# Optimization experiments

Hardware: AMD Instinct MI355X
Metric: run time of the kernel (lower is better)

Reference implementation:

```python
import jax, jax.numpy as jnp
import numpy as np

# Static module config (must match init_kwargs / input_specs)
C, HEADS, POINTS, LEVELS = 256, 8, 8, 2
H, W = 128, 128           # BEV grid per agent/level
NQ = H * W                # num_query = H*W
DH = C // HEADS           # per-head dim


def setup_inputs() -> dict:
    key = jax.random.key(0)
    ks = jax.random.split(key, 12)
    s = 0.02
    return {
        "query": jax.random.normal(ks[0], (1, NQ, C), jnp.float32),
        "query_pos": jax.random.normal(ks[1], (1, NQ, C), jnp.float32),
        "value": jax.random.normal(ks[2], (LEVELS, NQ, C), jnp.float32),
        "reference_points": jax.random.uniform(ks[3], (1, NQ, LEVELS, 2), jnp.float32),
        "spatial_shapes": jnp.full((LEVELS, 2), H, dtype=jnp.int32),
        "W_off": jax.random.normal(ks[4], (C, LEVELS * HEADS * POINTS * 2), jnp.float32) * s,
        "b_off": jax.random.normal(ks[5], (LEVELS * HEADS * POINTS * 2,), jnp.float32) * s,
        "W_attn": jax.random.normal(ks[6], (C, LEVELS * HEADS * POINTS), jnp.float32) * s,
        "b_attn": jax.random.normal(ks[7], (LEVELS * HEADS * POINTS,), jnp.float32) * s,
        "W_val": jax.random.normal(ks[8], (C, C), jnp.float32) * s,
        "b_val": jax.random.normal(ks[9], (C,), jnp.float32) * s,
        "W_out": jax.random.normal(ks[10], (C, C), jnp.float32) * s,
        "b_out": jax.random.normal(ks[11], (C,), jnp.float32) * s,
    }


def _bilinear(img, x, y):
    """grid_sample-style bilinear, align_corners=False, zero padding.
    img: (H, W, D); x, y: (...) pixel-space coords. Returns (..., D)."""
    Hh, Ww = img.shape[0], img.shape[1]
    x0f, y0f = jnp.floor(x), jnp.floor(y)
    x0, y0 = x0f.astype(jnp.int32), y0f.astype(jnp.int32)
    x1, y1 = x0 + 1, y0 + 1
    wx1, wy1 = x - x0f, y - y0f
    wx0, wy0 = 1.0 - wx1, 1.0 - wy1

    def gather(yy, xx):
        valid = (yy >= 0) & (yy < Hh) & (xx >= 0) & (xx < Ww)
        g = img[jnp.clip(yy, 0, Hh - 1), jnp.clip(xx, 0, Ww - 1)]
        return jnp.where(valid[..., None], g, 0.0)

    return (gather(y0, x0) * (wy0 * wx0)[..., None]
            + gather(y0, x1) * (wy0 * wx1)[..., None]
            + gather(y1, x0) * (wy1 * wx0)[..., None]
            + gather(y1, x1) * (wy1 * wx1)[..., None])


_sample_heads = jax.vmap(_bilinear, in_axes=(0, 0, 0))  # over heads


def reference(query, query_pos, value, reference_points, spatial_shapes,
              W_off, b_off, W_attn, b_attn, W_val, b_val, W_out, b_out):
    identity = query                                        # (1, NQ, C)
    q = (query + query_pos)[0]                              # (NQ, C), bs=1

    v = value @ W_val + b_val                               # (L, NQ, C)
    v = v.reshape(LEVELS, H, W, HEADS, DH)                  # per-level feature maps

    off = (q @ W_off + b_off).reshape(NQ, HEADS, LEVELS, POINTS, 2)
    attn = (q @ W_attn + b_attn).reshape(NQ, HEADS, LEVELS * POINTS)
    attn = jax.nn.softmax(attn, axis=-1).reshape(NQ, HEADS, LEVELS, POINTS)

    # offset_normalizer = (W, H) per level
    norm = jnp.stack([spatial_shapes[:, 1], spatial_shapes[:, 0]], -1).astype(q.dtype)  # (L, 2)
    # sampling_locations in normalized [0,1] coords: (NQ, HEADS, LEVELS, POINTS, 2)
    loc = reference_points[0][:, None, :, None, :] + off / norm[None, None, :, None, :]

    out = jnp.zeros((NQ, HEADS, DH), dtype=q.dtype)
    for l in range(LEVELS):
        img_l = jnp.transpose(v[l], (2, 0, 1, 3))           # (HEADS, H, W, DH)
        # align_corners=False: px = x_norm * W - 0.5
        xl = jnp.transpose(loc[:, :, l, :, 0], (1, 0, 2)) * W - 0.5  # (HEADS, NQ, POINTS)
        yl = jnp.transpose(loc[:, :, l, :, 1], (1, 0, 2)) * H - 0.5
        sampled = _sample_heads(img_l, xl, yl)              # (HEADS, NQ, POINTS, DH)
        out = out + jnp.einsum('hqpd,qhp->qhd', sampled, attn[:, :, l, :])

    out = out.reshape(NQ, C) @ W_out + b_out                # (NQ, C)
    return out[None] + identity                             # dropout is identity (eval / p=0)
```

## Files before the change

kernel.cpp:

```cpp
#include <hip/hip_runtime.h>
#include <hip/hip_bf16.h>
#include <math.h>

#define NQ     16384
#define CDIM   256
#define NHEADS 8
#define NPTS   8
#define NLVL   2
#define HH     128
#define WWID   128
#define DHEAD  32
#define NCAT   384

typedef __bf16 bf16_t;
typedef __bf16 bf16x8 __attribute__((ext_vector_type(8)));
typedef float  f32x4  __attribute__((ext_vector_type(4)));

typedef __attribute__((address_space(1))) const uint32_t gau32;
typedef __attribute__((address_space(3))) uint32_t lau32;

__device__ __forceinline__ bf16_t f2b(float f) { return (bf16_t)f; }

__global__ __launch_bounds__(256) void wtrans_all_k(const float* __restrict__ W_val,
                                                    const float* __restrict__ W_off,
                                                    const float* __restrict__ W_attn,
                                                    const float* __restrict__ W_out,
                                                    bf16_t* __restrict__ Wt_val,
                                                    bf16_t* __restrict__ Wt_qa,
                                                    bf16_t* __restrict__ Wt_out) {
    const int b = blockIdx.x;
    const float* W; bf16_t* Wt; int N, base;
    if (b < 256)      { W = W_val;  Wt = Wt_val;            N = 256; base = 0;   }
    else if (b < 512) { W = W_off;  Wt = Wt_qa;             N = 256; base = 256; }
    else if (b < 640) { W = W_attn; Wt = Wt_qa + 256 * 256; N = 128; base = 512; }
    else              { W = W_out;  Wt = Wt_out;            N = 256; base = 640; }
    int i = (b - base) * 256 + threadIdx.x;
    int n = i >> 8, k = i & 255;
    if (n >= N) return;
    Wt[i] = f2b(W[(size_t)k * N + n]);
}

template <int A_MODE, bool OUT_BF16, bool ADD_SRC, bool PERM_V>
__device__ __forceinline__ void gemm_body(bf16_t (&As)[128][64], bf16_t (&Bs)[128][64],
                                          int bidx, int bidy,
                                          const void* __restrict__ Aptr,
                                          const void* __restrict__ Aptr2,
                                          const bf16_t* __restrict__ Bt,
                                          const float* __restrict__ bias,
                                          const float* __restrict__ bias2,
                                          int Nsplit,
                                          const float* __restrict__ addsrc,
                                          void* __restrict__ Cout,
                                          int N, int K) {
    const int tid  = threadIdx.x;
    const int wave = tid >> 6;
    const int lane = tid & 63;
    const int rowBase = bidy * 128;
    const int colBase = bidx * 128;
    const int wm = (wave & 1) * 64;
    const int wn = (wave >> 1) * 64;
    const int fr = lane & 15;
    const int fq = lane >> 4;

    f32x4 acc[4][4] = {};

    const int lrow = lane >> 3;
    const int scol = ((lane & 7) ^ lrow) * 8;

    for (int k0 = 0; k0 < K; k0 += 64) {
        __syncthreads();
        if (A_MODE != 0) {
            const int r = tid >> 1, c = tid & 1;
            const float* ap = (const float*)Aptr + (size_t)(rowBase + r) * K + k0 + c * 32;
            const float* ap2 = (A_MODE == 2)
                ? (const float*)Aptr2 + (size_t)(rowBase + r) * K + k0 + c * 32 : nullptr;
#pragma unroll
            for (int u = 0; u < 4; ++u) {
                float4 f0 = *reinterpret_cast<const float4*>(ap + u * 8);
                float4 f1 = *reinterpret_cast<const float4*>(ap + u * 8 + 4);
                if (A_MODE == 2) {
                    float4 g0 = *reinterpret_cast<const float4*>(ap2 + u * 8);
                    float4 g1 = *reinterpret_cast<const float4*>(ap2 + u * 8 + 4);
                    f0.x += g0.x; f0.y += g0.y; f0.z += g0.z; f0.w += g0.w;
                    f1.x += g1.x; f1.y += g1.y; f1.z += g1.z; f1.w += g1.w;
                }
                bf16x8 bv;
                bv[0] = f2b(f0.x); bv[1] = f2b(f0.y); bv[2] = f2b(f0.z); bv[3] = f2b(f0.w);
                bv[4] = f2b(f1.x); bv[5] = f2b(f1.y); bv[6] = f2b(f1.z); bv[7] = f2b(f1.w);
                const int gp = ((c * 4 + u) ^ (r & 7)) * 8;
                *reinterpret_cast<bf16x8*>(&As[r][gp]) = bv;
            }
        } else {
            const bf16_t* Abf = (const bf16_t*)Aptr;
#pragma unroll
            for (int t = 0; t < 4; ++t) {
                const bf16_t* src =
                    Abf + (size_t)(rowBase + wave * 32 + t * 8 + lrow) * K + k0 + scol;
                __builtin_amdgcn_global_load_lds((gau32*)src,
                                                 (lau32*)&As[wave * 32 + t * 8][0],
                                                 16, 0, 0);
            }
        }
#pragma unroll
        for (int t = 0; t < 4; ++t) {
            const bf16_t* src =
                Bt + (size_t)(colBase + wave * 32 + t * 8 + lrow) * K + k0 + scol;
            __builtin_amdgcn_global_load_lds((gau32*)src,
                                             (lau32*)&Bs[wave * 32 + t * 8][0],
                                             16, 0, 0);
        }
        __syncthreads();
#pragma unroll
        for (int ks = 0; ks < 2; ++ks) {
            const int gk = ((ks * 4 + fq) ^ (fr & 7)) * 8;
            bf16x8 af[4], bfr[4];
#pragma unroll
            for (int i = 0; i < 4; ++i)
                af[i] = *reinterpret_cast<const bf16x8*>(&As[wm + i * 16 + fr][gk]);
#pragma unroll
            for (int j = 0; j < 4; ++j)
                bfr[j] = *reinterpret_cast<const bf16x8*>(&Bs[wn + j * 16 + fr][gk]);
#pragma unroll
            for (int i = 0; i < 4; ++i)
#pragma unroll
                for (int j = 0; j < 4; ++j)
                    acc[i][j] = __builtin_amdgcn_mfma_f32_16x16x32_bf16(af[i], bfr[j],
                                                                        acc[i][j], 0, 0, 0);
        }
    }

#pragma unroll
    for (int j = 0; j < 4; ++j) {
        const int col = colBase + wn + j * 16 + fr;
        const float bv = (col < Nsplit) ? bias[col] : bias2[col - Nsplit];
#pragma unroll
        for (int i = 0; i < 4; ++i) {
#pragma unroll
            for (int r = 0; r < 4; ++r) {
                const int row = rowBase + wm + i * 16 + fq * 4 + r;
                float vv = acc[i][j][r] + bv;
                if (ADD_SRC) vv += addsrc[(size_t)row * N + col];
                if (PERM_V) {
                    const int l = row >> 14, cell = row & 16383;
                    const size_t dst =
                        (((size_t)(l * NHEADS + (col >> 5)) * NQ + cell) << 5) + (col & 31);
                    ((bf16_t*)Cout)[dst] = f2b(vv);
                } else if (OUT_BF16) {
                    ((bf16_t*)Cout)[(size_t)row * N + col] = f2b(vv);
                } else {
                    ((float*)Cout)[(size_t)row * N + col] = vv;
                }
            }
        }
    }
}

__global__ __launch_bounds__(256, 3) void fused_proj_k(const float* __restrict__ value,
                                                       const float* __restrict__ query,
                                                       const float* __restrict__ query_pos,
                                                       const bf16_t* __restrict__ Wt_val,
                                                       const bf16_t* __restrict__ Wt_qa,
                                                       const float* __restrict__ b_val,
                                                       const float* __restrict__ b_off,
                                                       const float* __restrict__ b_attn,
                                                       bf16_t* __restrict__ v2,
                                                       float* __restrict__ cbuf) {
    __shared__ __align__(16) bf16_t As[128][64];
    __shared__ __align__(16) bf16_t Bs[128][64];
    const int b = blockIdx.x;
    if (b < 512) {
        const int bidy = (b >> 4) * 8 + (b & 7);
        const int bidx = (b >> 3) & 1;
        gemm_body<1, true, false, true>(As, Bs, bidx, bidy, value, nullptr,
                                        Wt_val, b_val, b_val, 256, nullptr, v2,
                                        CDIM, CDIM);
    } else {
        const int b2 = b - 512;
        const int bidy = (b2 / 24) * 8 + (b2 & 7);
        const int bidx = (b2 >> 3) % 3;
        gemm_body<2, false, false, false>(As, Bs, bidx, bidy, query, query_pos,
                                          Wt_qa, b_off, b_attn, 256, nullptr, cbuf,
                                          NCAT, CDIM);
    }
}

__global__ __launch_bounds__(256, 3) void outproj_k(const bf16_t* __restrict__ tmp,
                                                    const bf16_t* __restrict__ Wt_out,
                                                    const float* __restrict__ b_out,
                                                    const float* __restrict__ query,
                                                    float* __restrict__ out) {
    __shared__ __align__(16) bf16_t As[128][64];
    __shared__ __align__(16) bf16_t Bs[128][64];
    const int b = blockIdx.x;
    const int bidy = (b >> 4) * 8 + (b & 7);
    const int bidx = (b >> 3) & 1;
    gemm_body<0, false, true, false>(As, Bs, bidx, bidy, tmp, nullptr,
                                     Wt_out, b_out, b_out, 256, query, out,
                                     CDIM, CDIM);
}

__global__ __launch_bounds__(256) void sample_k(const bf16_t* __restrict__ v2,
                                                const float* __restrict__ cbuf,
                                                const float* __restrict__ refp,
                                                bf16_t* __restrict__ tmp) {
    const int b    = blockIdx.x;
    const int h    = b & 7;
    const int qblk = b >> 3;
    const int tid  = threadIdx.x;
    const int qloc = tid >> 2;
    const int ck   = tid & 3;
    const int q    = qblk * 64 + qloc;

    const float* qrow = cbuf + (size_t)q * NCAT;
    const float4 rp = *reinterpret_cast<const float4*>(refp + (size_t)q * 4);

    const float* attp = qrow + 256 + h * 16;
    float4 A0 = *reinterpret_cast<const float4*>(attp);
    float4 A1 = *reinterpret_cast<const float4*>(attp + 4);
    float4 A2 = *reinterpret_cast<const float4*>(attp + 8);
    float4 A3 = *reinterpret_cast<const float4*>(attp + 12);
    float e[16] = {A0.x, A0.y, A0.z, A0.w, A1.x, A1.y, A1.z, A1.w,
                   A2.x, A2.y, A2.z, A2.w, A3.x, A3.y, A3.z, A3.w};
    float m = e[0];
#pragma unroll
    for (int i = 1; i < 16; ++i) m = fmaxf(m, e[i]);
    float s = 0.f;
#pragma unroll
    for (int i = 0; i < 16; ++i) { e[i] = __expf(e[i] - m); s += e[i]; }
    const float inv = 1.f / s;
#pragma unroll
    for (int i = 0; i < 16; ++i) e[i] *= inv;

    float acc[8] = {0.f, 0.f, 0.f, 0.f, 0.f, 0.f, 0.f, 0.f};

#pragma unroll
    for (int l = 0; l < NLVL; ++l) {
        const float bx = (l == 0 ? rp.x : rp.z) * (float)WWID - 0.5f;
        const float by = (l == 0 ? rp.y : rp.w) * (float)HH - 0.5f;
        const bf16_t* base = v2 + ((size_t)(l * NHEADS + h) * NQ) * DHEAD + ck * 8;
        const float* offp  = qrow + h * 32 + l * 16;

        float4 o0 = *reinterpret_cast<const float4*>(offp);
        float4 o1 = *reinterpret_cast<const float4*>(offp + 4);
        float4 o2 = *reinterpret_cast<const float4*>(offp + 8);
        float4 o3 = *reinterpret_cast<const float4*>(offp + 12);
        const float ox[8] = {o0.x, o0.z, o1.x, o1.z, o2.x, o2.z, o3.x, o3.z};
        const float oy[8] = {o0.y, o0.w, o1.y, o1.w, o2.y, o2.w, o3.y, o3.w};

#pragma unroll
        for (int p = 0; p < NPTS; ++p) {
            const float px = bx + ox[p];
            const float py = by + oy[p];
            const float w  = e[l * 8 + p];
            const float x0f = floorf(px), y0f = floorf(py);
            const int x0 = (int)x0f, y0 = (int)y0f;
            const float wx1 = px - x0f, wy1 = py - y0f;
            const float wx0 = 1.f - wx1, wy0 = 1.f - wy1;
            const bool vx0 = (unsigned)x0 < (unsigned)WWID;
            const bool vx1 = (unsigned)(x0 + 1) < (unsigned)WWID;
            const bool vy0 = (unsigned)y0 < (unsigned)HH;
            const bool vy1 = (unsigned)(y0 + 1) < (unsigned)HH;
            const int xc0 = min(max(x0, 0), WWID - 1);
            const int xc1 = min(max(x0 + 1, 0), WWID - 1);
            const int yc0 = min(max(y0, 0), HH - 1);
            const int yc1 = min(max(y0 + 1, 0), HH - 1);
            const bf16_t* r0 = base + yc0 * (WWID * DHEAD);
            const bf16_t* r1 = base + yc1 * (WWID * DHEAD);
            bf16x8 v00 = *reinterpret_cast<const bf16x8*>(r0 + xc0 * DHEAD);
            bf16x8 v10 = *reinterpret_cast<const bf16x8*>(r0 + xc1 * DHEAD);
            bf16x8 v01 = *reinterpret_cast<const bf16x8*>(r1 + xc0 * DHEAD);
            bf16x8 v11 = *reinterpret_cast<const bf16x8*>(r1 + xc1 * DHEAD);
            const float w00 = (vx0 & vy0) ? w * wx0 * wy0 : 0.f;
            const float w10 = (vx1 & vy0) ? w * wx1 * wy0 : 0.f;
            const float w01 = (vx0 & vy1) ? w * wx0 * wy1 : 0.f;
            const float w11 = (vx1 & vy1) ? w * wx1 * wy1 : 0.f;
#pragma unroll
            for (int i = 0; i < 8; ++i) {
                acc[i] = fmaf(w00, (float)v00[i], acc[i]);
                acc[i] = fmaf(w10, (float)v10[i], acc[i]);
                acc[i] = fmaf(w01, (float)v01[i], acc[i]);
                acc[i] = fmaf(w11, (float)v11[i], acc[i]);
            }
        }
    }

    bf16x8 ov;
#pragma unroll
    for (int i = 0; i < 8; ++i) ov[i] = f2b(acc[i]);
    *reinterpret_cast<bf16x8*>(tmp + (size_t)q * CDIM + h * DHEAD + ck * 8) = ov;
}

extern "C" void kernel_launch(void* const* d_in, const int* in_sizes, int n_in,
                              void* d_out, int out_size, void* d_ws, size_t ws_size,
                              hipStream_t stream) {
    const float* query     = (const float*)d_in[0];
    const float* query_pos = (const float*)d_in[1];
    const float* value     = (const float*)d_in[2];
    const float* refp      = (const float*)d_in[3];
    const float* W_off  = (const float*)d_in[5];
    const float* b_off  = (const float*)d_in[6];
    const float* W_attn = (const float*)d_in[7];
    const float* b_attn = (const float*)d_in[8];
    const float* W_val  = (const float*)d_in[9];
    const float* b_val  = (const float*)d_in[10];
    const float* W_out  = (const float*)d_in[11];
    const float* b_out  = (const float*)d_in[12];
    float* out = (float*)d_out;

    char* ws = (char*)d_ws;
    bf16_t* v2      = (bf16_t*)(ws);
    float*  cbuf    = (float*)(ws + 16777216);
    bf16_t* tmp     = (bf16_t*)(ws + 41943040);
    bf16_t* Wt_val  = (bf16_t*)(ws + 50331648);
    bf16_t* Wt_qa   = (bf16_t*)(ws + 50462720);
    bf16_t* Wt_out  = (bf16_t*)(ws + 50659328);

    wtrans_all_k<<<896, 256, 0, stream>>>(W_val, W_off, W_attn, W_out,
                                          Wt_val, Wt_qa, Wt_out);
    fused_proj_k<<<896, 256, 0, stream>>>(value, query, query_pos,
                                          Wt_val, Wt_qa, b_val, b_off, b_attn,
                                          v2, cbuf);
    sample_k<<<2048, 256, 0, stream>>>(v2, cbuf, refp, tmp);
    outproj_k<<<256, 256, 0, stream>>>(tmp, Wt_out, b_out, query, out);
}
```

Before: 211.3 us.

## Store value maps as zero-padded fp8 and sample without bounds masks

Projected value maps are now written as fp8 into a 130x130 zero-padded grid per level/head, so sampling only clamps coordinates to [-1,128] and drops the per-tap validity masks. Gathers read 8 bytes instead of 16 and use packed fp8-to-f32 conversions with vector accumulation. The weight transpose kernel now uses an LDS-tiled transpose and also zeroes the padded buffer. Storing values in fp8 instead of bf16 costs precision, and the odd-byte scattered writes in the GEMM epilogue may be inefficient.

Result: faster. 197.4 us (-6.6%).

```diff
diff --git a/kernel.cpp b/kernel.cpp
--- a/kernel.cpp
+++ b/kernel.cpp
@@ -12,32 +12,55 @@
 #define DHEAD  32
 #define NCAT   384
 
+#define PW        130
+#define CELLB     32
+#define ROWB      (PW * CELLB)
+#define MAPB      (PW * PW * CELLB)
+#define V2BYTES   (NLVL * NHEADS * MAPB)
+#define MEMSET_BLKS 2113
+
 typedef __bf16 bf16_t;
 typedef __bf16 bf16x8 __attribute__((ext_vector_type(8)));
 typedef float  f32x4  __attribute__((ext_vector_type(4)));
+typedef float  f32x2  __attribute__((ext_vector_type(2)));
 
 typedef __attribute__((address_space(1))) const uint32_t gau32;
 typedef __attribute__((address_space(3))) uint32_t lau32;
 
 __device__ __forceinline__ bf16_t f2b(float f) { return (bf16_t)f; }
 
-__global__ __launch_bounds__(256) void wtrans_all_k(const float* __restrict__ W_val,
-                                                    const float* __restrict__ W_off,
-                                                    const float* __restrict__ W_attn,
-                                                    const float* __restrict__ W_out,
-                                                    bf16_t* __restrict__ Wt_val,
-                                                    bf16_t* __restrict__ Wt_qa,
-                                                    bf16_t* __restrict__ Wt_out) {
+__global__ __launch_bounds__(256) void prep_k(const float* __restrict__ W_val,
+                                              const float* __restrict__ W_off,
+                                              const float* __restrict__ W_attn,
+                                              const float* __restrict__ W_out,
+                                              unsigned char* __restrict__ v2,
+                                              bf16_t* __restrict__ Wt_val,
+                                              bf16_t* __restrict__ Wt_qa,
+                                              bf16_t* __restrict__ Wt_out) {
     const int b = blockIdx.x;
-    const float* W; bf16_t* Wt; int N, base;
-    if (b < 256)      { W = W_val;  Wt = Wt_val;            N = 256; base = 0;   }
-    else if (b < 512) { W = W_off;  Wt = Wt_qa;             N = 256; base = 256; }
-    else if (b < 640) { W = W_attn; Wt = Wt_qa + 256 * 256; N = 128; base = 512; }
-    else              { W = W_out;  Wt = Wt_out;            N = 256; base = 640; }
-    int i = (b - base) * 256 + threadIdx.x;
-    int n = i >> 8, k = i & 255;
-    if (n >= N) return;
-    Wt[i] = f2b(W[(size_t)k * N + n]);
+    if (b < MEMSET_BLKS) {
+        size_t off = ((size_t)b * 256 + threadIdx.x) * 16;
+        if (off < V2BYTES)
+            *reinterpret_cast<uint4*>(v2 + off) = make_uint4(0, 0, 0, 0);
+        return;
+    }
+    const int tb = b - MEMSET_BLKS;
+    const float* W; bf16_t* Wt; int N, t;
+    if (tb < 64)       { W = W_val;  Wt = Wt_val;            N = 256; t = tb;       }
+    else if (tb < 128) { W = W_off;  Wt = Wt_qa;             N = 256; t = tb - 64;  }
+    else if (tb < 160) { W = W_attn; Wt = Wt_qa + 256 * 256; N = 128; t = tb - 128; }
+    else               { W = W_out;  Wt = Wt_out;            N = 256; t = tb - 160; }
+    const int ntn = N >> 5;
+    const int k0 = (t / ntn) * 32, n0 = (t % ntn) * 32;
+    const int tx = threadIdx.x & 31, ty = threadIdx.x >> 5;
+    __shared__ float s[32][33];
+#pragma unroll
+    for (int i = 0; i < 4; ++i)
+        s[ty + 8 * i][tx] = W[(size_t)(k0 + ty + 8 * i) * N + n0 + tx];
+    __syncthreads();
+#pragma unroll
+    for (int i = 0; i < 4; ++i)
+        Wt[(size_t)(n0 + ty + 8 * i) * 256 + k0 + tx] = f2b(s[tx][ty + 8 * i]);
 }
 
 template <int A_MODE, bool OUT_BF16, bool ADD_SRC, bool PERM_V>
@@ -142,9 +165,12 @@
                 if (ADD_SRC) vv += addsrc[(size_t)row * N + col];
                 if (PERM_V) {
                     const int l = row >> 14, cell = row & 16383;
-                    const size_t dst =
-                        (((size_t)(l * NHEADS + (col >> 5)) * NQ + cell) << 5) + (col & 31);
-                    ((bf16_t*)Cout)[dst] = f2b(vv);
+                    const int y = cell >> 7, x = cell & 127;
+                    const size_t dst = (size_t)(l * NHEADS + (col >> 5)) * MAPB
+                                     + (size_t)(y + 1) * ROWB + (x + 1) * CELLB
+                                     + (col & 31);
+                    const uint32_t pk = __builtin_amdgcn_cvt_pk_fp8_f32(vv, vv, 0, false);
+                    ((unsigned char*)Cout)[dst] = (unsigned char)(pk & 0xff);
                 } else if (OUT_BF16) {
                     ((bf16_t*)Cout)[(size_t)row * N + col] = f2b(vv);
                 } else {
@@ -163,7 +189,7 @@
                                                        const float* __restrict__ b_val,
                                                        const float* __restrict__ b_off,
                                                        const float* __restrict__ b_attn,
-                                                       bf16_t* __restrict__ v2,
+                                                       unsigned char* __restrict__ v2,
                                                        float* __restrict__ cbuf) {
     __shared__ __align__(16) bf16_t As[128][64];
     __shared__ __align__(16) bf16_t Bs[128][64];
@@ -199,7 +225,14 @@
                                      CDIM, CDIM);
 }
 
-__global__ __launch_bounds__(256) void sample_k(const bf16_t* __restrict__ v2,
+__device__ __forceinline__ void acc_tap(uint2 u, float w, f32x2* acc2) {
+    acc2[0] += __builtin_amdgcn_cvt_pk_f32_fp8((int)u.x, false) * w;
+    acc2[1] += __builtin_amdgcn_cvt_pk_f32_fp8((int)u.x, true)  * w;
+    acc2[2] += __builtin_amdgcn_cvt_pk_f32_fp8((int)u.y, false) * w;
+    acc2[3] += __builtin_amdgcn_cvt_pk_f32_fp8((int)u.y, true)  * w;
+}
+
+__global__ __launch_bounds__(256) void sample_k(const unsigned char* __restrict__ v2,
                                                 const float* __restrict__ cbuf,
                                                 const float* __restrict__ refp,
                                                 bf16_t* __restrict__ tmp) {
@@ -231,14 +264,15 @@
 #pragma unroll
     for (int i = 0; i < 16; ++i) e[i] *= inv;
 
-    float acc[8] = {0.f, 0.f, 0.f, 0.f, 0.f, 0.f, 0.f, 0.f};
+    f32x2 acc2[4] = {{0.f, 0.f}, {0.f, 0.f}, {0.f, 0.f}, {0.f, 0.f}};
 
 #pragma unroll
     for (int l = 0; l < NLVL; ++l) {
         const float bx = (l == 0 ? rp.x : rp.z) * (float)WWID - 0.5f;
         const float by = (l == 0 ? rp.y : rp.w) * (float)HH - 0.5f;
-        const bf16_t* base = v2 + ((size_t)(l * NHEADS + h) * NQ) * DHEAD + ck * 8;
-        const float* offp  = qrow + h * 32 + l * 16;
+        const unsigned char* base = v2 + (size_t)(l * NHEADS + h) * MAPB
+                                       + 131 * CELLB + ck * 8;
+        const float* offp = qrow + h * 32 + l * 16;
 
         float4 o0 = *reinterpret_cast<const float4*>(offp);
         float4 o1 = *reinterpret_cast<const float4*>(offp + 4);
@@ -256,37 +290,30 @@
             const int x0 = (int)x0f, y0 = (int)y0f;
             const float wx1 = px - x0f, wy1 = py - y0f;
             const float wx0 = 1.f - wx1, wy0 = 1.f - wy1;
-            const bool vx0 = (unsigned)x0 < (unsigned)WWID;
-            const bool vx1 = (unsigned)(x0 + 1) < (unsigned)WWID;
-            const bool vy0 = (unsigned)y0 < (unsigned)HH;
-            const bool vy1 = (unsigned)(y0 + 1) < (unsigned)HH;
-            const int xc0 = min(max(x0, 0), WWID - 1);
-            const int xc1 = min(max(x0 + 1, 0), WWID - 1);
-            const int yc0 = min(max(y0, 0), HH - 1);
-            const int yc1 = min(max(y0 + 1, 0), HH - 1);
-            const bf16_t* r0 = base + yc0 * (WWID * DHEAD);
-            const bf16_t* r1 = base + yc1 * (WWID * DHEAD);
-            bf16x8 v00 = *reinterpret_cast<const bf16x8*>(r0 + xc0 * DHEAD);
-            bf16x8 v10 = *reinterpret_cast<const bf16x8*>(r0 + xc1 * DHEAD);
-            bf16x8 v01 = *reinterpret_cast<const bf16x8*>(r1 + xc0 * DHEAD);
-            bf16x8 v11 = *reinterpret_cast<const bf16x8*>(r1 + xc1 * DHEAD);
-            const float w00 = (vx0 & vy0) ? w * wx0 * wy0 : 0.f;
-            const float w10 = (vx1 & vy0) ? w * wx1 * wy0 : 0.f;
-            const float w01 = (vx0 & vy1) ? w * wx0 * wy1 : 0.f;
-            const float w11 = (vx1 & vy1) ? w * wx1 * wy1 : 0.f;
-#pragma unroll
-            for (int i = 0; i < 8; ++i) {
-                acc[i] = fmaf(w00, (float)v00[i], acc[i]);
-                acc[i] = fmaf(w10, (float)v10[i], acc[i]);
-                acc[i] = fmaf(w01, (float)v01[i], acc[i]);
-                acc[i] = fmaf(w11, (float)v11[i], acc[i]);
-            }
+            const int x0c = min(max(x0, -1), 128);
+            const int x1c = min(max(x0 + 1, -1), 128);
+            const int y0c = min(max(y0, -1), 128);
+            const int y1c = min(max(y0 + 1, -1), 128);
+            const unsigned char* r0 = base + y0c * ROWB;
+            const unsigned char* r1 = base + y1c * ROWB;
+            uint2 u00 = *reinterpret_cast<const uint2*>(r0 + x0c * CELLB);
+            uint2 u10 = *reinterpret_cast<const uint2*>(r0 + x1c * CELLB);
+            uint2 u01 = *reinterpret_cast<const uint2*>(r1 + x0c * CELLB);
+            uint2 u11 = *reinterpret_cast<const uint2*>(r1 + x1c * CELLB);
+            const float wy0w = w * wy0, wy1w = w * wy1;
+            acc_tap(u00, wy0w * wx0, acc2);
+            acc_tap(u10, wy0w * wx1, acc2);
+            acc_tap(u01, wy1w * wx0, acc2);
+            acc_tap(u11, wy1w * wx1, acc2);
         }
     }
 
     bf16x8 ov;
 #pragma unroll
-    for (int i = 0; i < 8; ++i) ov[i] = f2b(acc[i]);
+    for (int i = 0; i < 4; ++i) {
+        ov[2 * i]     = f2b(acc2[i].x);
+        ov[2 * i + 1] = f2b(acc2[i].y);
+    }
     *reinterpret_cast<bf16x8*>(tmp + (size_t)q * CDIM + h * DHEAD + ck * 8) = ov;
 }
 
@@ -308,15 +335,15 @@
     float* out = (float*)d_out;
 
     char* ws = (char*)d_ws;
-    bf16_t* v2      = (bf16_t*)(ws);
-    float*  cbuf    = (float*)(ws + 16777216);
-    bf16_t* tmp     = (bf16_t*)(ws + 41943040);
-    bf16_t* Wt_val  = (bf16_t*)(ws + 50331648);
-    bf16_t* Wt_qa   = (bf16_t*)(ws + 50462720);
-    bf16_t* Wt_out  = (bf16_t*)(ws + 50659328);
-
-    wtrans_all_k<<<896, 256, 0, stream>>>(W_val, W_off, W_attn, W_out,
-                                          Wt_val, Wt_qa, Wt_out);
+    unsigned char* v2 = (unsigned char*)(ws);
+    float*  cbuf    = (float*)(ws + 8654848);
+    bf16_t* tmp     = (bf16_t*)(ws + 33820672);
+    bf16_t* Wt_val  = (bf16_t*)(ws + 42209280);
+    bf16_t* Wt_qa   = (bf16_t*)(ws + 42340352);
+    bf16_t* Wt_out  = (bf16_t*)(ws + 42536960);
+
+    prep_k<<<MEMSET_BLKS + 224, 256, 0, stream>>>(W_val, W_off, W_attn, W_out,
+                                                  v2, Wt_val, Wt_qa, Wt_out);
     fused_proj_k<<<896, 256, 0, stream>>>(value, query, query_pos,
                                           Wt_val, Wt_qa, b_val, b_off, b_attn,
                                           v2, cbuf);
```
